# Kernel optimization log

Hardware: AMD Instinct MI355X
Metric: run time of the kernel (lower is better)

## Reference

```python
import jax, jax.numpy as jnp
import numpy as np

EPS = 1e-5  # torch BatchNorm default


def setup_inputs() -> dict:
    key = jax.random.key(0)
    k1, k2, k3 = jax.random.split(key, 3)
    N, C, T, V, O = 64, 64, 300, 25, 64
    x = jax.random.normal(k1, (N, C, T, V), dtype=jnp.float32)
    # 24 = V-1 convs, each (O, C, 1, 2) -> packed as (V-1, O, C, 2), scaled like conv_init
    W = jax.random.normal(k2, (V - 1, O, C, 2), dtype=jnp.float32) * (1.0 / np.sqrt(2 * C))
    b = jax.random.normal(k3, (V - 1, O), dtype=jnp.float32) * 0.01
    gamma = jnp.ones((O,), dtype=jnp.float32)
    beta = jnp.zeros((O,), dtype=jnp.float32)
    return {"x": x, "W": W, "b": b, "gamma": gamma, "beta": beta}


def reference(x, W, b, gamma, beta):
    # x: (N, C, T, V); W: (V-1, O, C, 2); b: (V-1, O)
    # Math of the original loop: out[..., v] = sum_i W0_i @ x[..., v]
    #   + sum_i W1_i @ x[..., (v+i+1) % V] + sum_i b_i
    V = x.shape[-1]
    W0 = W[..., 0]  # (V-1, O, C)
    W1 = W[..., 1]  # (V-1, O, C)
    # identity-tap term: all W0 share the same column -> sum once
    S0 = W0.sum(axis=0)  # (O, C)
    out = jnp.einsum('oc,nctv->notv', S0, x)
    # circular term: source u = (v+i+1)%V  <=>  i = (u-v-1)%V, valid for u != v
    v_idx = jnp.arange(V)
    off = (v_idx[None, :] - v_idx[:, None] - 1) % V  # (V_target, V_source) -> i, equals V-1 when u==v
    W1p = jnp.concatenate([W1, jnp.zeros_like(W1[:1])], axis=0)  # index V-1 maps to zero (u==v excluded)
    Wg = W1p[off]  # (V, V, O, C), zero on the diagonal
    out = out + jnp.einsum('vuoc,nctu->notv', Wg, x)
    out = out + b.sum(axis=0)[None, :, None, None]
    # BatchNorm2d (training-mode batch stats, biased variance) + ReLU
    mean = out.mean(axis=(0, 2, 3), keepdims=True)
    var = out.var(axis=(0, 2, 3), keepdims=True)
    out = (out - mean) * jax.lax.rsqrt(var + EPS)
    out = out * gamma[None, :, None, None] + beta[None, :, None, None]
    return jax.nn.relu(out)
```

## Files before the change

### kernel.cpp

```cpp
#include <hip/hip_runtime.h>


typedef short  s16x8 __attribute__((ext_vector_type(8)));
typedef float  f32x4 __attribute__((ext_vector_type(4)));

#define NTHR_   256
#define RPB_    250
#define NBR_    30
#define TS_     260

__device__ __forceinline__ unsigned short f2bf(float f) {
  unsigned u = __builtin_bit_cast(unsigned, f);
  return (unsigned short)((u + 0x7FFFu + ((u >> 16) & 1u)) >> 16);
}

__global__ void pack_w_kernel(const float* __restrict__ W, s16x8* __restrict__ Wg) {
  int idx = blockIdx.x * 256 + threadIdx.x;
  if (idx >= 12800) return;
  int lane  = idx & 63;
  int ni    = (idx >> 6) & 3;
  int chunk = (idx >> 8) & 1;
  int s     = idx >> 9;
  int o     = (ni << 4) + (lane & 15);
  int cbase = (chunk << 5) + ((lane >> 4) << 3);
  s16x8 h;
#pragma unroll
  for (int j = 0; j < 8; ++j) {
    int c = cbase + j;
    float val;
    if (s == 0) {
      val = 0.f;
      for (int i = 0; i < 24; ++i) val += W[((i * 64 + o) * 64 + c) * 2];
    } else {
      val = W[(((s - 1) * 64 + o) * 64 + c) * 2 + 1];
    }
    h[j] = (short)f2bf(val);
  }
  Wg[idx] = h;
}

#define ADV(J) { bool w_ = (u[J] == 24); u[J] = w_ ? 0 : u[J] + 1; \
                 aoc[J] += w_ ? -384 : 16; }
#define MM(RT, CT, AF, BF) \
  acc[RT][CT] = __builtin_amdgcn_mfma_f32_16x16x32_bf16(AF, BF, acc[RT][CT], 0, 0, 0);

#define SHIFT(S_, BB)                                                          \
  {                                                                            \
    int sc_ = (S_) + 2; sc_ = (sc_ > 24) ? 24 : sc_;                           \
    const s16x8* ws_ = Wg + sc_ * 512;                                         \
    s16x8 Br0_ = ws_[tid], Br1_ = ws_[256 + tid];                              \
    const char* bq_ = Bsh + (BB) * 8192 + 4096 + (lane << 4);                  \
    __builtin_amdgcn_s_setprio(1);                                             \
    Aq0 = *(const s16x8*)(Ash + aoc[0] + 16384);                               \
    MM(0, 0, Ap0, Bp0) MM(0, 1, Ap0, Bp1)                                      \
    Bq0 = *(const s16x8*)(bq_);                                                \
    MM(0, 2, Ap0, Bp2) MM(0, 3, Ap0, Bp3)                                      \
    Aq1 = *(const s16x8*)(Ash + aoc[1] + 16384);                               \
    MM(1, 0, Ap1, Bp0) MM(1, 1, Ap1, Bp1)                                      \
    Bq1 = *(const s16x8*)(bq_ + 1024);                                         \
    MM(1, 2, Ap1, Bp2) MM(1, 3, Ap1, Bp3)                                      \
    Aq2 = *(const s16x8*)(Ash + aoc[2] + 16384);                               \
    MM(2, 0, Ap2, Bp0) MM(2, 1, Ap2, Bp1)                                      \
    Bq2 = *(const s16x8*)(bq_ + 2048);                                         \
    MM(2, 2, Ap2, Bp2) MM(2, 3, Ap2, Bp3)                                      \
    Aq3 = *(const s16x8*)(Ash + aoc[3] + 16384);                               \
    MM(3, 0, Ap3, Bp0) MM(3, 1, Ap3, Bp1)                                      \
    Bq3 = *(const s16x8*)(bq_ + 3072);                                         \
    MM(3, 2, Ap3, Bp2) MM(3, 3, Ap3, Bp3)                                      \
    __builtin_amdgcn_s_setprio(0);                                             \
    __syncthreads();                                                           \
    const char* bp_ = Bsh + (((BB) ^ 1) * 8192) + (lane << 4);                 \
    __builtin_amdgcn_s_setprio(1);                                             \
    ADV(0) Ap0 = *(const s16x8*)(Ash + aoc[0]);                                \
    MM(0, 0, Aq0, Bq0) MM(0, 1, Aq0, Bq1)                                      \
    Bp0 = *(const s16x8*)(bp_);                                                \
    MM(0, 2, Aq0, Bq2) MM(0, 3, Aq0, Bq3)                                      \
    ADV(1) Ap1 = *(const s16x8*)(Ash + aoc[1]);                                \
    MM(1, 0, Aq1, Bq0) MM(1, 1, Aq1, Bq1)                                      \
    Bp1 = *(const s16x8*)(bp_ + 1024);                                         \
    MM(1, 2, Aq1, Bq2) MM(1, 3, Aq1, Bq3)                                      \
    ADV(2) Ap2 = *(const s16x8*)(Ash + aoc[2]);                                \
    MM(2, 0, Aq2, Bq0) MM(2, 1, Aq2, Bq1)                                      \
    Bp2 = *(const s16x8*)(bp_ + 2048);                                         \
    MM(2, 2, Aq2, Bq2) MM(2, 3, Aq2, Bq3)                                      \
    ADV(3) Ap3 = *(const s16x8*)(Ash + aoc[3]);                                \
    MM(3, 0, Aq3, Bq0) MM(3, 1, Aq3, Bq1)                                      \
    Bp3 = *(const s16x8*)(bp_ + 3072);                                         \
    MM(3, 2, Aq3, Bq2) MM(3, 3, Aq3, Bq3)                                      \
    __builtin_amdgcn_s_setprio(0);                                             \
    *(s16x8*)(Bsh + (BB) * 8192 + (tid << 4)) = Br0_;                          \
    *(s16x8*)(Bsh + (BB) * 8192 + 4096 + (tid << 4)) = Br1_;                   \
  }

__global__ __launch_bounds__(NTHR_) void tap_mm_kernel(
    const float* __restrict__ x, const s16x8* __restrict__ Wg,
    float* __restrict__ out, float* __restrict__ partials) {
  __shared__ __align__(16) char Ash[32768];
  __shared__ __align__(16) char Bsh[16384];
  __shared__ float red2[512];
  int br = blockIdx.x, n = blockIdx.y;
  int r0 = br * RPB_;
  const float* xn = x + n * 480000 + r0;
  int tid = threadIdx.x;
  int wid = tid >> 6, lane = tid & 63;
  int l15 = lane & 15, lk = lane >> 4;

  s16x8 p0 = Wg[tid], p1 = Wg[256 + tid], p2 = Wg[512 + tid], p3 = Wg[768 + tid];

#pragma unroll 2
  for (int it = 0; it < 8; ++it) {
    bool vld = tid < RPB_;
    s16x8 h;
#pragma unroll
    for (int j = 0; j < 8; ++j) {
      float f = vld ? xn[((it << 3) + j) * 7500 + tid] : 0.f;
      h[j] = (short)f2bf(f);
    }
    *(s16x8*)(Ash + (it << 12) + (tid << 4)) = h;
  }
  *(s16x8*)(Bsh + (tid << 4))         = p0;
  *(s16x8*)(Bsh + 4096 + (tid << 4))  = p1;
  *(s16x8*)(Bsh + 8192 + (tid << 4))  = p2;
  *(s16x8*)(Bsh + 12288 + (tid << 4)) = p3;

  int u[4], aoc[4];
#pragma unroll
  for (int rt = 0; rt < 4; ++rt) {
    int srow = (wid << 6) + (rt << 4) + l15;
    u[rt]   = srow % 25;
    aoc[rt] = (lk << 12) + (srow << 4);
  }
  f32x4 acc[4][4];
#pragma unroll
  for (int rt = 0; rt < 4; ++rt)
#pragma unroll
    for (int ct = 0; ct < 4; ++ct) acc[rt][ct] = (f32x4){0.f, 0.f, 0.f, 0.f};

  __syncthreads();

  s16x8 Ap0 = *(const s16x8*)(Ash + aoc[0]);
  s16x8 Ap1 = *(const s16x8*)(Ash + aoc[1]);
  s16x8 Ap2 = *(const s16x8*)(Ash + aoc[2]);
  s16x8 Ap3 = *(const s16x8*)(Ash + aoc[3]);
  const char* b0_ = Bsh + (lane << 4);
  s16x8 Bp0 = *(const s16x8*)(b0_);
  s16x8 Bp1 = *(const s16x8*)(b0_ + 1024);
  s16x8 Bp2 = *(const s16x8*)(b0_ + 2048);
  s16x8 Bp3 = *(const s16x8*)(b0_ + 3072);
  s16x8 Aq0, Aq1, Aq2, Aq3, Bq0, Bq1, Bq2, Bq3;

  for (int k = 0; k < 12; ++k) {
    SHIFT(2 * k, 0)
    SHIFT(2 * k + 1, 1)
  }
  SHIFT(24, 0)

  float s1v[4] = {0.f, 0.f, 0.f, 0.f}, s2v[4] = {0.f, 0.f, 0.f, 0.f};
#pragma unroll
  for (int rt = 0; rt < 4; ++rt) {
#pragma unroll
    for (int qq = 0; qq < 4; ++qq) {
      int rloc = (wid << 6) + (rt << 4) + (lk << 2) + qq;
      if (rloc < RPB_) {
#pragma unroll
        for (int ct = 0; ct < 4; ++ct) {
          float val = acc[rt][ct][qq];
          s1v[ct] += val;
          s2v[ct] += val * val;
        }
      }
    }
  }
#pragma unroll
  for (int ct = 0; ct < 4; ++ct) {
    float a = s1v[ct], b = s2v[ct];
    a += __shfl_xor(a, 16); a += __shfl_xor(a, 32);
    b += __shfl_xor(b, 16); b += __shfl_xor(b, 32);
    if (lane < 16) {
      int base = ((((wid << 2) + ct) << 4) + l15) * 2;
      red2[base]     = a;
      red2[base + 1] = b;
    }
  }

  float* T = (float*)Ash;
  float* outb = out + n * 480000 + r0;
#pragma unroll
  for (int qt = 0; qt < 4; ++qt) {
    __syncthreads();
#pragma unroll
    for (int rt = 0; rt < 4; ++rt) {
      int row0 = (wid << 6) + (rt << 4) + (lk << 2);
      *(f32x4*)&T[l15 * TS_ + row0] = acc[rt][qt];
    }
    __syncthreads();
    if (qt == 0 && tid < 128) {
      int o = tid >> 1, m = tid & 1;
      int ct = o >> 4, ol = o & 15;
      float sres = 0.f;
#pragma unroll
      for (int w = 0; w < 4; ++w)
        sres += red2[((((w << 2) + ct) << 4) + ol) * 2 + m];
      int bl = n * NBR_ + br;
      partials[bl * 128 + m * 64 + o] = sres;
    }
#pragma unroll
    for (int it = 0; it < 8; ++it) {
      int idx = tid + it * NTHR_;
      if (idx < 2000) {
        int ol = idx / 125, r2 = idx - ol * 125;
        *(float2*)&outb[((qt << 4) + ol) * 7500 + (r2 << 1)] =
            *(float2*)&T[ol * TS_ + (r2 << 1)];
      }
    }
  }
}

__global__ void finalize_kernel(const float* __restrict__ part,
                                const float* __restrict__ gamma,
                                const float* __restrict__ beta,
                                float* __restrict__ scsh) {
  __shared__ float sm[512];
  int o = blockIdx.x;
  int tid = threadIdx.x;
  float s1 = 0.f, s2 = 0.f;
  for (int b = tid; b < 64 * NBR_; b += 256) {
    s1 += part[b * 128 + o];
    s2 += part[b * 128 + 64 + o];
  }
  sm[tid] = s1; sm[256 + tid] = s2;
  __syncthreads();
  for (int st = 128; st >= 1; st >>= 1) {
    if (tid < st) { sm[tid] += sm[tid + st]; sm[256 + tid] += sm[256 + tid + st]; }
    __syncthreads();
  }
  if (tid == 0) {
    const float inv = 1.0f / 480000.0f;
    float mean = sm[0] * inv;
    float var  = sm[256] * inv - mean * mean;
    float sc = gamma[o] * rsqrtf(var + 1e-5f);
    float sh = beta[o] - mean * sc;
    scsh[o]      = sc;
    scsh[64 + o] = sh;
  }
}

__global__ void bn_relu_kernel(float4* __restrict__ out, const float* __restrict__ scsh) {
  int i = blockIdx.x * blockDim.x + threadIdx.x;
  const int total = 7680000;
  int stride = gridDim.x * blockDim.x;
  for (; i < total; i += stride) {
    int o = (i / 1875) & 63;
    float sc = scsh[o], sh = scsh[64 + o];
    float4 v = out[i];
    v.x = fmaxf(fmaf(v.x, sc, sh), 0.f);
    v.y = fmaxf(fmaf(v.y, sc, sh), 0.f);
    v.z = fmaxf(fmaf(v.z, sc, sh), 0.f);
    v.w = fmaxf(fmaf(v.w, sc, sh), 0.f);
    out[i] = v;
  }
}

extern "C" void kernel_launch(void* const* d_in, const int* in_sizes, int n_in,
                              void* d_out, int out_size, void* d_ws, size_t ws_size,
                              hipStream_t stream) {
  const float* x     = (const float*)d_in[0];
  const float* W     = (const float*)d_in[1];
  const float* gamma = (const float*)d_in[3];
  const float* beta  = (const float*)d_in[4];
  float* out = (float*)d_out;

  char* ws = (char*)d_ws;
  s16x8* Wg       = (s16x8*)ws;
  float* partials = (float*)(ws + 204800);
  float* scsh     = (float*)(ws + 204800 + 983040);

  pack_w_kernel<<<dim3(50), dim3(256), 0, stream>>>(W, Wg);
  tap_mm_kernel<<<dim3(NBR_, 64), dim3(NTHR_), 0, stream>>>(x, Wg, out, partials);
  finalize_kernel<<<dim3(64), dim3(256), 0, stream>>>(partials, gamma, beta, scsh);
  bn_relu_kernel<<<dim3(2048), dim3(256), 0, stream>>>((float4*)out, scsh);
}
```

Baseline: 180.8 us.

## Stream weight tiles into LDS with async global_load_lds and triple buffering

Weight tiles are no longer loaded through registers and stored to LDS. They are fetched with global-to-LDS direct loads into a triple-buffered B ring, and each step prefetches two shifts ahead. The full __syncthreads is replaced by a vmcnt wait plus a raw s_barrier. This is meant to cut register pressure and ds_write traffic and to overlap weight fetches with MFMA work. The cost is extra LDS space, which may lower occupancy, and it relies on exact waitcnt accounting being correct.

```diff
diff --git a/kernel.cpp b/kernel.cpp
--- a/kernel.cpp
+++ b/kernel.cpp
@@ -13,6 +13,11 @@
   unsigned u = __builtin_bit_cast(unsigned, f);
   return (unsigned short)((u + 0x7FFFu + ((u >> 16) & 1u)) >> 16);
 }
+
+#define GLDS16(G, L)                                                           \
+  __builtin_amdgcn_global_load_lds(                                            \
+      (const __attribute__((address_space(1))) void*)(G),                      \
+      (__attribute__((address_space(3))) void*)(L), 16, 0, 0);
 
 __global__ void pack_w_kernel(const float* __restrict__ W, s16x8* __restrict__ Wg) {
   int idx = blockIdx.x * 256 + threadIdx.x;
@@ -44,12 +49,13 @@
 #define MM(RT, CT, AF, BF) \
   acc[RT][CT] = __builtin_amdgcn_mfma_f32_16x16x32_bf16(AF, BF, acc[RT][CT], 0, 0, 0);
 
-#define SHIFT(S_, BB)                                                          \
+#define SHIFT(S_, CUR, NXT, FUT)                                               \
   {                                                                            \
-    int sc_ = (S_) + 2; sc_ = (sc_ > 24) ? 24 : sc_;                           \
-    const s16x8* ws_ = Wg + sc_ * 512;                                         \
-    s16x8 Br0_ = ws_[tid], Br1_ = ws_[256 + tid];                              \
-    const char* bq_ = Bsh + (BB) * 8192 + 4096 + (lane << 4);                  \
+    int sq_ = (S_) + 2; sq_ = (sq_ > 24) ? 24 : sq_;                           \
+    const char* g_ = (const char*)(Wg + sq_ * 512) + goff;                     \
+    GLDS16(g_,        Bsh + (FUT) * 8192 + loff)                               \
+    GLDS16(g_ + 1024, Bsh + (FUT) * 8192 + loff + 1024)                        \
+    const char* bq_ = Bsh + (CUR) * 8192 + 4096 + (lane << 4);                 \
     __builtin_amdgcn_s_setprio(1);                                             \
     Aq0 = *(const s16x8*)(Ash + aoc[0] + 16384);                               \
     MM(0, 0, Ap0, Bp0) MM(0, 1, Ap0, Bp1)                                      \
@@ -68,8 +74,10 @@
     Bq3 = *(const s16x8*)(bq_ + 3072);                                         \
     MM(3, 2, Ap3, Bp2) MM(3, 3, Ap3, Bp3)                                      \
     __builtin_amdgcn_s_setprio(0);                                             \
-    __syncthreads();                                                           \
-    const char* bp_ = Bsh + (((BB) ^ 1) * 8192) + (lane << 4);                 \
+    asm volatile("s_waitcnt vmcnt(2)" ::: "memory");                           \
+    __builtin_amdgcn_s_barrier();                                              \
+    __builtin_amdgcn_sched_barrier(0);                                         \
+    const char* bp_ = Bsh + (NXT) * 8192 + (lane << 4);                        \
     __builtin_amdgcn_s_setprio(1);                                             \
     ADV(0) Ap0 = *(const s16x8*)(Ash + aoc[0]);                                \
     MM(0, 0, Aq0, Bq0) MM(0, 1, Aq0, Bq1)                                      \
@@ -88,15 +96,13 @@
     Bp3 = *(const s16x8*)(bp_ + 3072);                                         \
     MM(3, 2, Aq3, Bq2) MM(3, 3, Aq3, Bq3)                                      \
     __builtin_amdgcn_s_setprio(0);                                             \
-    *(s16x8*)(Bsh + (BB) * 8192 + (tid << 4)) = Br0_;                          \
-    *(s16x8*)(Bsh + (BB) * 8192 + 4096 + (tid << 4)) = Br1_;                   \
   }
 
 __global__ __launch_bounds__(NTHR_) void tap_mm_kernel(
     const float* __restrict__ x, const s16x8* __restrict__ Wg,
     float* __restrict__ out, float* __restrict__ partials) {
   __shared__ __align__(16) char Ash[32768];
-  __shared__ __align__(16) char Bsh[16384];
+  __shared__ __align__(16) char Bsh[24576];
   __shared__ float red2[512];
   int br = blockIdx.x, n = blockIdx.y;
   int r0 = br * RPB_;
@@ -104,8 +110,17 @@
   int tid = threadIdx.x;
   int wid = tid >> 6, lane = tid & 63;
   int l15 = lane & 15, lk = lane >> 4;
-
-  s16x8 p0 = Wg[tid], p1 = Wg[256 + tid], p2 = Wg[512 + tid], p3 = Wg[768 + tid];
+  int goff = (wid << 11) + (lane << 4);
+  int loff = (wid << 11);
+
+  {
+    const char* g0 = (const char*)Wg + goff;
+    GLDS16(g0,        Bsh + loff)
+    GLDS16(g0 + 1024, Bsh + loff + 1024)
+    const char* g1 = (const char*)(Wg + 512) + goff;
+    GLDS16(g1,        Bsh + 8192 + loff)
+    GLDS16(g1 + 1024, Bsh + 8192 + loff + 1024)
+  }
 
 #pragma unroll 2
   for (int it = 0; it < 8; ++it) {
@@ -118,10 +133,6 @@
     }
     *(s16x8*)(Ash + (it << 12) + (tid << 4)) = h;
   }
-  *(s16x8*)(Bsh + (tid << 4))         = p0;
-  *(s16x8*)(Bsh + 4096 + (tid << 4))  = p1;
-  *(s16x8*)(Bsh + 8192 + (tid << 4))  = p2;
-  *(s16x8*)(Bsh + 12288 + (tid << 4)) = p3;
 
   int u[4], aoc[4];
 #pragma unroll
@@ -149,11 +160,15 @@
   s16x8 Bp3 = *(const s16x8*)(b0_ + 3072);
   s16x8 Aq0, Aq1, Aq2, Aq3, Bq0, Bq1, Bq2, Bq3;
 
-  for (int k = 0; k < 12; ++k) {
-    SHIFT(2 * k, 0)
-    SHIFT(2 * k + 1, 1)
-  }
-  SHIFT(24, 0)
+  for (int base = 0; base < 24; base += 6) {
+    SHIFT(base + 0, 0, 1, 2)
+    SHIFT(base + 1, 1, 2, 0)
+    SHIFT(base + 2, 2, 0, 1)
+    SHIFT(base + 3, 0, 1, 2)
+    SHIFT(base + 4, 1, 2, 0)
+    SHIFT(base + 5, 2, 0, 1)
+  }
+  SHIFT(24, 0, 1, 2)
 
   float s1v[4] = {0.f, 0.f, 0.f, 0.f}, s2v[4] = {0.f, 0.f, 0.f, 0.f};
 #pragma unroll
```

Measured after the change: 179.3 us. Within noise of the previous version (-0.8%).
